# Kernel optimization log

Hardware: AMD Instinct MI355X
Metric: run time of the kernel (lower is better)

Reference implementation:

```python
import jax, jax.numpy as jnp
import numpy as np

D_MODEL, D_STATE, EXPAND = 1024, 128, 2
E = D_MODEL * EXPAND          # 2048
N = D_STATE                   # 128
H = 1
P = E
TD = D_STATE // 2             # 64
Z_DIM = E + E + N + N + H + H + TD + H  # 4369
EPS = 1e-05
B_SZ, L = 4, 2048


def setup_inputs() -> dict:
    key = jax.random.key(0)
    ks = jax.random.split(key, 6)
    u = jax.random.normal(ks[0], (B_SZ, L, D_MODEL), dtype=jnp.float32)
    W_in = jax.random.normal(ks[1], (Z_DIM, D_MODEL), dtype=jnp.float32) * 0.02
    W_out = jax.random.normal(ks[2], (D_MODEL, E), dtype=jnp.float32) * 0.02
    w_normB = jnp.ones((N,), jnp.float32)
    w_normC = jnp.ones((N,), jnp.float32)
    B_bias = jnp.ones((N,), jnp.float32)
    C_bias = jnp.ones((N,), jnp.float32)
    # dt_bias buffer: dt_i ~ logU(0.001, 0.1); dt_bias = dt_i + log(-expm1(-dt_i))
    dt_i = jnp.exp(jax.random.uniform(ks[3], (H,)) * (np.log(0.1) - np.log(0.001)) + np.log(0.001))
    dt_i = jnp.clip(dt_i, 1e-4, None)
    dt_bias = dt_i + jnp.log(-jnp.expm1(-dt_i))
    A_log = jnp.full((H,), np.log(0.5), jnp.float32)
    return {"u": u, "W_in": W_in, "w_normB": w_normB, "w_normC": w_normC,
            "B_bias": B_bias, "C_bias": C_bias, "dt_bias": dt_bias,
            "A_log": A_log, "W_out": W_out}


def _rms(x, w):
    return x * jax.lax.rsqrt(jnp.mean(x * x, axis=-1, keepdims=True) + EPS) * w


def _rope(x, ang):
    half = x.shape[-1] // 2
    x1, x2 = x[..., :half], x[..., half:]
    c, s = jnp.cos(ang), jnp.sin(ang)
    return jnp.concatenate([x1 * c - x2 * s, x1 * s + x2 * c], axis=-1)


def reference(u, W_in, w_normB, w_normC, B_bias, C_bias, dt_bias, A_log, W_out):
    Bb, Ls, _ = u.shape
    z = u @ W_in.T  # [B, L, Z_DIM]
    o = 0
    def take(n):
        nonlocal o
        r = z[..., o:o + n]; o += n; return r
    x = jax.nn.silu(take(E))
    gate = jax.nn.silu(take(E))
    B_ = take(N)
    C_ = take(N)
    dt_ = take(H)
    A_ = take(H)
    th = take(TD)
    lam_ = take(H)

    dt = jax.nn.softplus(dt_ + dt_bias)          # [B, L, H]
    A = -jax.nn.softplus(A_ + A_log)             # [B, L, H]
    lam = jax.nn.sigmoid(lam_)                   # [B, L, H]
    alpha = jnp.exp(dt * A)                      # [B, L, H]

    B_ = _rms(B_, w_normB) + B_bias
    C_ = _rms(C_, w_normC) + C_bias
    ca = jnp.cumsum(jnp.mean(dt, axis=-1, keepdims=True) * th, axis=1)  # [B, L, TD]
    B_ = _rope(B_, ca)
    C_ = _rope(C_, ca)

    xh = x.reshape(Bb, Ls, H, P)
    xp = jnp.concatenate([jnp.zeros_like(xh[:, :1]), xh[:, :-1]], axis=1)  # roll + zero t=0
    lh = lam[..., None]
    xt = lh * xh + (1.0 - lh) * alpha[..., None] * xp  # [B, L, H, P]

    # fallback SSM: per-channel mean drive, per-head scalar A (mean over batch+time)
    u_mean = jnp.mean(xt, axis=-1)               # [B, L, H]
    A_bar = jnp.mean(A, axis=(0, 1))             # [H]
    dA = jnp.exp(dt * A_bar)                     # [B, L, H]
    dBu = dt[..., None] * B_[:, :, None, :] * u_mean[..., None]  # [B, L, H, N]

    def step(state, xs):
        dA_t, dBu_t, C_t = xs                    # [B,H], [B,H,N], [B,N]
        state = dA_t[..., None] * state + dBu_t  # [B, H, N]
        y_t = jnp.einsum('bhn,bn->bh', state, C_t)
        return state, y_t

    state0 = jnp.zeros((Bb, H, N), dtype=xt.dtype)
    _, ys = jax.lax.scan(step, state0,
                         (jnp.moveaxis(dA, 1, 0), jnp.moveaxis(dBu, 1, 0), jnp.moveaxis(C_, 1, 0)))
    outs = jnp.moveaxis(ys, 0, 1)                # [B, L, H]
    y = jnp.broadcast_to(outs, (Bb, Ls, E))      # H=1 expanded to E
    return (y * gate) @ W_out.T
```

## Files before the change

kernel.cpp:

```cpp
#include <hip/hip_runtime.h>
#include <cstdint>
#include <cstddef>

typedef __bf16 bf16_t;
typedef bf16_t bf16x8 __attribute__((ext_vector_type(8)));
typedef bf16_t bf16x4 __attribute__((ext_vector_type(4)));
typedef float f32x4 __attribute__((ext_vector_type(4)));

#define B_SZ    4
#define LSEQ    2048
#define DMODEL  1024
#define EDIM    2048
#define ZDIM    4419
#define ZPAD    4608
#define ROWS    (B_SZ*LSEQ)
#define EPSV    1e-5f

#define LDU     1088
#define LDG     2112

#define SCHUNK  128
#define SCLEN   (LSEQ/SCHUNK)
#define RCH     128
#define RCLEN   (LSEQ/RCH)

__device__ __forceinline__ float softplus_f(float x){
  return fmaxf(x, 0.f) + log1pf(expf(-fabsf(x)));
}
__device__ __forceinline__ float sigmoid_f(float x){ return 1.f/(1.f+expf(-x)); }
__device__ __forceinline__ float silu_f(float x){ return x/(1.f+expf(-x)); }

__device__ __forceinline__ void gload_lds16(const void* g, void* l){
  __builtin_amdgcn_global_load_lds(
      (const __attribute__((address_space(1))) void*)g,
      (__attribute__((address_space(3))) void*)l, 16, 0, 0);
}

__device__ __forceinline__ float blockReduce128(float v, float* red, int t){
  red[t] = v; __syncthreads();
  #pragma unroll
  for (int off = 64; off > 0; off >>= 1){
    if (t < off) red[t] += red[t+off];
    __syncthreads();
  }
  float r = red[0];
  __syncthreads();
  return r;
}

__global__ __launch_bounds__(256) void prep_kernel(
    const float4* __restrict__ u4, const float4* __restrict__ win4,
    const float4* __restrict__ wout4,
    bf16_t* __restrict__ ubf, bf16_t* __restrict__ winSh, bf16_t* __restrict__ woutSh,
    float* __restrict__ Asum, float* __restrict__ xraw)
{
  size_t i = (size_t)blockIdx.x*256 + threadIdx.x;
  if (i == 0) Asum[0] = 0.f;
  if (i < ROWS) xraw[i] = 0.f;
  const size_t NU4 = (size_t)ROWS*DMODEL/4;
  const size_t NW4 = (size_t)ZPAD*DMODEL/4;
  const size_t NO4 = (size_t)DMODEL*EDIM/4;
  if (i < NU4){
    float4 v = u4[i];
    size_t e = i*4, row = e>>10, col = e&1023;
    bf16x4 o = { (bf16_t)v.x, (bf16_t)v.y, (bf16_t)v.z, (bf16_t)v.w };
    *(bf16x4*)&ubf[row*LDU + col] = o;
    return;
  }
  i -= NU4;
  if (i < NW4){
    size_t e = i*4, row = e>>10, k = e&1023;
    bf16x4 o;
    if (row < (size_t)ZDIM){
      float4 v = win4[i];
      o = bf16x4{ (bf16_t)v.x, (bf16_t)v.y, (bf16_t)v.z, (bf16_t)v.w };
    } else {
      o = bf16x4{ (bf16_t)0.f, (bf16_t)0.f, (bf16_t)0.f, (bf16_t)0.f };
    }
    int ntile = (int)(row>>4), colf = (int)(row&15);
    int kt = (int)(k>>5), koct = (int)((k>>3)&3), ko = (int)(k&7);
    size_t off = (((size_t)ntile*32 + kt)<<9) + (koct<<7) + (colf<<3) + ko;
    *(bf16x4*)&winSh[off] = o;
    return;
  }
  i -= NW4;
  if (i < NO4){
    float4 v = wout4[i];
    size_t e = i*4, row = e>>11, k = e&2047;
    bf16x4 o = { (bf16_t)v.x, (bf16_t)v.y, (bf16_t)v.z, (bf16_t)v.w };
    int ntile = (int)(row>>4), colf = (int)(row&15);
    int kt = (int)(k>>5), koct = (int)((k>>3)&3), ko = (int)(k&7);
    size_t off = (((size_t)ntile*64 + kt)<<9) + (koct<<7) + (colf<<3) + ko;
    *(bf16x4*)&woutSh[off] = o;
  }
}

template<int LDA_, int NKT, int NT, int NXT, int MODE>
__global__ __launch_bounds__(256, 2) void gemmV_kernel(
    const bf16_t* __restrict__ A0, const bf16_t* __restrict__ Bsh,
    float* __restrict__ xraw, bf16_t* __restrict__ o_g, float* __restrict__ o_z,
    const float* __restrict__ scale, float* __restrict__ o_f)
{
  __shared__ __align__(16) bf16_t lds[8192];

  const int tid = threadIdx.x;
  const int wid = tid>>6, lane = tid&63;
  const int wr = wid>>1, wc = wid&1;
  const int lr = lane&15, hi = lane>>4;

  constexpr int MB = ROWS/128;
  constexpr int NWG = NXT*MB;
  const int id = blockIdx.x;
  const int rid = (id & 7)*(NWG/8) + (id>>3);
  const int bx = rid % NXT, by = rid / NXT;
  const int m0 = by*128, n0 = bx*256;

  f32x4 acc[4][8] = {};

  const bf16_t* pA0; const bf16_t* pA1;
  int dA0, dA1;
  {
    int c0 = tid,      r0 = c0>>2, d0 = c0&3, g0 = (d0 - (r0>>1)) & 3;
    int c1 = 256+tid,  r1 = c1>>2, d1 = c1&3, g1 = (d1 - (r1>>1)) & 3;
    pA0 = A0 + (size_t)(m0+r0)*LDA_ + g0*8;
    pA1 = A0 + (size_t)(m0+r1)*LDA_ + g1*8;
    dA0 = c0*8; dA1 = c1*8;
  }
  int aoff[4];
  {
    int R0 = wr*64 + lr;
    int cA = (hi + (R0>>1)) & 3;
    #pragma unroll
    for (int m = 0; m < 4; ++m) aoff[m] = (R0 + 16*m)*32 + cA*8;
  }
  const bf16_t* bB0 = Bsh + (((size_t)((n0>>4) + wc*8)*NKT)<<9) + lane*8;
  int koff = 0;

  bf16x8 bA[8], bB[8], af[4];

  gload_lds16(pA0, &lds[dA0]); pA0 += 32;
  gload_lds16(pA1, &lds[dA1]); pA1 += 32;
  #pragma unroll
  for (int n = 0; n < 8; ++n)
    bA[n] = *(const bf16x8*)(bB0 + (size_t)n*(NKT*512) + koff);
  koff += 512;
  asm volatile("s_waitcnt vmcnt(8)" ::: "memory");
  __builtin_amdgcn_s_barrier();

  #pragma unroll 1
  for (int t2 = 0; t2 < NT/2; ++t2){
    {
      #pragma unroll
      for (int m = 0; m < 4; ++m) af[m] = *(const bf16x8*)&lds[aoff[m]];
      gload_lds16(pA0, &lds[4096 + dA0]); pA0 += 32;
      gload_lds16(pA1, &lds[4096 + dA1]); pA1 += 32;
      #pragma unroll
      for (int n = 0; n < 8; ++n)
        bB[n] = *(const bf16x8*)(bB0 + (size_t)n*(NKT*512) + koff);
      koff += 512;
      #pragma unroll
      for (int m = 0; m < 4; ++m)
        #pragma unroll
        for (int n = 0; n < 8; ++n)
          acc[m][n] = __builtin_amdgcn_mfma_f32_16x16x32_bf16(af[m], bA[n], acc[m][n], 0,0,0);
      asm volatile("s_waitcnt vmcnt(8)" ::: "memory");
      __builtin_amdgcn_s_barrier();
    }
    {
      #pragma unroll
      for (int m = 0; m < 4; ++m) af[m] = *(const bf16x8*)&lds[4096 + aoff[m]];
      const bool pf = (t2 < NT/2 - 1);
      if (pf){
        gload_lds16(pA0, &lds[dA0]); pA0 += 32;
        gload_lds16(pA1, &lds[dA1]); pA1 += 32;
        #pragma unroll
        for (int n = 0; n < 8; ++n)
          bA[n] = *(const bf16x8*)(bB0 + (size_t)n*(NKT*512) + koff);
        koff += 512;
      }
      #pragma unroll
      for (int m = 0; m < 4; ++m)
        #pragma unroll
        for (int n = 0; n < 8; ++n)
          acc[m][n] = __builtin_amdgcn_mfma_f32_16x16x32_bf16(af[m], bB[n], acc[m][n], 0,0,0);
      if (pf) { asm volatile("s_waitcnt vmcnt(8)" ::: "memory"); }
      else    { asm volatile("s_waitcnt vmcnt(0)" ::: "memory"); }
      __builtin_amdgcn_s_barrier();
    }
  }

  if (MODE == 0 && n0 < 2048){
    #pragma unroll
    for (int m = 0; m < 4; ++m){
      #pragma unroll
      for (int i = 0; i < 4; ++i){
        float p = 0.f;
        #pragma unroll
        for (int n = 0; n < 8; ++n) p += silu_f(acc[m][n][i]);
        p += __shfl_xor(p, 8); p += __shfl_xor(p, 4);
        p += __shfl_xor(p, 2); p += __shfl_xor(p, 1);
        if (lr == 0){
          int r = m0 + wr*64 + m*16 + (hi<<2) + i;
          atomicAdd(xraw + r, p);
        }
      }
    }
  } else if (MODE == 0){
    #pragma unroll
    for (int m = 0; m < 4; ++m){
      int rowb = m0 + wr*64 + m*16 + (hi<<2);
      #pragma unroll
      for (int n = 0; n < 8; ++n){
        int col = n0 + wc*128 + n*16 + lr;
        #pragma unroll
        for (int i = 0; i < 4; ++i){
          int r = rowb + i;
          float v = acc[m][n][i];
          if (col < 4096)      o_g[(size_t)r*LDG + (col-2048)] = (bf16_t)silu_f(v);
          else if (col < 4480) o_z[(size_t)r*384 + (col-4096)] = v;
        }
      }
    }
  } else {
    #pragma unroll
    for (int m = 0; m < 4; ++m){
      int rowb = m0 + wr*64 + m*16 + (hi<<2);
      #pragma unroll
      for (int i = 0; i < 4; ++i){
        int r = rowb + i;
        float s = scale[r];
        #pragma unroll
        for (int n = 0; n < 8; ++n){
          int col = n0 + wc*128 + n*16 + lr;
          o_f[(size_t)r*DMODEL + col] = acc[m][n][i]*s;
        }
      }
    }
  }
}

__global__ __launch_bounds__(128) void fuse_kernel(
    const float* __restrict__ xraw, const float* __restrict__ zs,
    const float* __restrict__ wnB, const float* __restrict__ wnC,
    const float* __restrict__ Bb, const float* __restrict__ Cb,
    const float* __restrict__ dtb, const float* __restrict__ Alog,
    float* __restrict__ Bn, float* __restrict__ Cn, float* __restrict__ dtth,
    float* __restrict__ dts, float* __restrict__ alphas, float* __restrict__ lams,
    float* __restrict__ xbar, float* Asum)
{
  __shared__ float red[128];
  int r = blockIdx.x, t = threadIdx.x;
  const float* zr = zs + (size_t)r*384;
  float bv = zr[t], cv = zr[128+t];
  float b2 = blockReduce128(bv*bv, red, t);
  float c2 = blockReduce128(cv*cv, red, t);
  float rb = rsqrtf(b2*(1.f/128.f) + EPSV);
  float rc = rsqrtf(c2*(1.f/128.f) + EPSV);
  Bn[(size_t)r*128 + t] = bv*rb*wnB[t] + Bb[t];
  Cn[(size_t)r*128 + t] = cv*rc*wnC[t] + Cb[t];

  float dt = softplus_f(zr[256] + dtb[0]);
  if (t < 64) dtth[(size_t)r*64 + t] = dt * zr[258+t];
  if (t == 0){
    float Av  = -softplus_f(zr[257] + Alog[0]);
    float lam = sigmoid_f(zr[322]);
    dts[r]    = dt;
    alphas[r] = expf(dt*Av);
    lams[r]   = lam;
    xbar[r]   = xraw[r] * (1.f/2048.f);
    atomicAdd(Asum, Av);
  }
}

__global__ __launch_bounds__(64) void rope_sum_kernel(
    const float* __restrict__ dtth, float* __restrict__ csum)
{
  int b  = blockIdx.x >> 7;
  int ch = blockIdx.x & 127;
  int d  = threadIdx.x;
  const float* base = dtth + ((size_t)b*LSEQ + (size_t)ch*RCLEN)*64 + d;
  float s = 0.f;
  #pragma unroll
  for (int i = 0; i < RCLEN; ++i) s += base[(size_t)i*64];
  csum[((size_t)b*RCH + ch)*64 + d] = s;
}

__global__ __launch_bounds__(64) void rope_prefix_kernel(float* __restrict__ csum)
{
  int b = blockIdx.x, d = threadIdx.x;
  float s = 0.f;
  for (int c = 0; c < RCH; ++c){
    size_t idx = ((size_t)b*RCH + c)*64 + d;
    float v = csum[idx]; csum[idx] = s; s += v;
  }
}

__global__ __launch_bounds__(64) void rope_scan_kernel(
    const float* __restrict__ dtth, const float* __restrict__ csum,
    const float* __restrict__ dts, const float* __restrict__ alphas,
    const float* __restrict__ lams, const float* __restrict__ xbar,
    const float* __restrict__ Asum,
    const float* __restrict__ Bn, float* __restrict__ Cn,
    float* __restrict__ ylocal, float* __restrict__ Pfix,
    float* __restrict__ Sfin, float* __restrict__ Dch)
{
  int b  = blockIdx.x >> 7;
  int ch = blockIdx.x & 127;
  int d  = threadIdx.x;
  float Abar = Asum[0] * (1.f/(float)ROWS);
  float ca = csum[((size_t)b*RCH + ch)*64 + d];
  float s1 = 0.f, s2 = 0.f, P = 1.f;
  int l0 = ch*SCLEN;
  #pragma unroll
  for (int i = 0; i < SCLEN; ++i){
    int l = l0 + i;
    size_t r = (size_t)b*LSEQ + l;
    ca += dtth[r*64 + d];
    float sn, cs;
    sincosf(ca, &sn, &cs);
    size_t ro = r*128;
    float b1 = Bn[ro+d], b2v = Bn[ro+64+d];
    float rb1 = b1*cs - b2v*sn;
    float rb2 = b1*sn + b2v*cs;
    float c1 = Cn[ro+d], c2v = Cn[ro+64+d];
    float rc1 = c1*cs - c2v*sn;
    float rc2 = c1*sn + c2v*cs;
    Cn[ro+d]    = rc1;
    Cn[ro+64+d] = rc2;

    float dt = dts[r], lam = lams[r], al = alphas[r], xb = xbar[r];
    float xp = (l > 0) ? xbar[r-1] : 0.f;
    float um = lam*xb + (1.f-lam)*al*xp;
    float dA = expf(dt*Abar);
    float coef = dt*um;
    s1 = dA*s1 + coef*rb1;
    s2 = dA*s2 + coef*rb2;
    P *= dA;
    float p = s1*rc1 + s2*rc2;
    #pragma unroll
    for (int off = 32; off > 0; off >>= 1) p += __shfl_down(p, off);
    if (d == 0){ ylocal[r] = p; Pfix[r] = P; }
  }
  size_t so = ((size_t)b*SCHUNK + ch)*128;
  Sfin[so + d]      = s1;
  Sfin[so + 64 + d] = s2;
  if (d == 0) Dch[b*SCHUNK + ch] = P;
}

__global__ __launch_bounds__(128) void scan_carry_kernel(
    const float* __restrict__ Sfin, const float* __restrict__ Dch,
    float* __restrict__ Sin)
{
  int b = blockIdx.x;
  int n = threadIdx.x;
  float s = 0.f;
  for (int c = 0; c < SCHUNK; ++c){
    size_t so = ((size_t)b*SCHUNK + c)*128;
    Sin[so + n] = s;
    s = Dch[b*SCHUNK + c]*s + Sfin[so + n];
  }
}

__global__ __launch_bounds__(256) void scan_fix_kernel(
    const float* __restrict__ Cn, const float* __restrict__ Sin,
    const float* __restrict__ ylocal, const float* __restrict__ Pfix,
    float* __restrict__ outsv)
{
  int r = blockIdx.x*4 + (threadIdx.x>>6);
  int n = threadIdx.x & 63;
  int b  = r / LSEQ;
  int ch = (r % LSEQ) / SCLEN;
  const float* si = Sin + ((size_t)b*SCHUNK + ch)*128;
  size_t ro = (size_t)r*128;
  float p = Cn[ro+n]*si[n] + Cn[ro+64+n]*si[64+n];
  #pragma unroll
  for (int off = 32; off > 0; off >>= 1) p += __shfl_down(p, off);
  if (n == 0) outsv[r] = ylocal[r] + Pfix[r]*p;
}

extern "C" void kernel_launch(void* const* d_in, const int* in_sizes, int n_in,
                              void* d_out, int out_size, void* d_ws, size_t ws_size,
                              hipStream_t stream)
{
  const float* u    = (const float*)d_in[0];
  const float* W_in = (const float*)d_in[1];
  const float* wnB  = (const float*)d_in[2];
  const float* wnC  = (const float*)d_in[3];
  const float* Bb   = (const float*)d_in[4];
  const float* Cb   = (const float*)d_in[5];
  const float* dtb  = (const float*)d_in[6];
  const float* Alog = (const float*)d_in[7];
  const float* Wout = (const float*)d_in[8];
  float* out = (float*)d_out;
  char* ws = (char*)d_ws;

  constexpr size_t OFF_ASUM = 0;
  constexpr size_t OFF_UBF  = 256;
  constexpr size_t SZ_UBF   = (size_t)ROWS*LDU*2;
  constexpr size_t OFF_WIN  = OFF_UBF + SZ_UBF;
  constexpr size_t SZ_WIN   = (size_t)ZPAD*LDU*2;
  constexpr size_t OFF_WOUT = OFF_WIN + SZ_WIN;
  constexpr size_t SZ_WOUT  = (size_t)DMODEL*LDG*2;
  constexpr size_t OFF_G    = OFF_WOUT + SZ_WOUT;
  constexpr size_t SZ_G     = (size_t)ROWS*LDG*2;
  constexpr size_t OFF_ZS   = OFF_G + SZ_G;
  constexpr size_t SZ_ZS    = (size_t)ROWS*384*4;
  constexpr size_t OFF_BN   = OFF_ZS + SZ_ZS;
  constexpr size_t SZ_BN    = (size_t)ROWS*128*4;
  constexpr size_t OFF_CN   = OFF_BN + SZ_BN;
  constexpr size_t OFF_DTTH = OFF_CN + SZ_BN;
  constexpr size_t SZ_DTTH  = (size_t)ROWS*64*4;
  constexpr size_t OFF_XRAW = OFF_DTTH + SZ_DTTH;
  constexpr size_t OFF_DT   = OFF_XRAW + (size_t)ROWS*4;
  constexpr size_t OFF_AL   = OFF_DT  + (size_t)ROWS*4;
  constexpr size_t OFF_LAM  = OFF_AL  + (size_t)ROWS*4;
  constexpr size_t OFF_XB   = OFF_LAM + (size_t)ROWS*4;
  constexpr size_t OFF_OUTS = OFF_XB  + (size_t)ROWS*4;
  constexpr size_t OFF_YLOC = OFF_OUTS + (size_t)ROWS*4;
  constexpr size_t OFF_PFIX = OFF_YLOC + (size_t)ROWS*4;
  constexpr size_t OFF_SFIN = OFF_PFIX + (size_t)ROWS*4;
  constexpr size_t SZ_SFIN  = (size_t)B_SZ*SCHUNK*128*4;
  constexpr size_t OFF_DCH  = OFF_SFIN + SZ_SFIN;
  constexpr size_t OFF_SIN  = OFF_DCH + (size_t)B_SZ*SCHUNK*4;
  constexpr size_t OFF_CSUM = OFF_SIN + SZ_SFIN;

  float*  Asum   = (float*) (ws + OFF_ASUM);
  bf16_t* ubf    = (bf16_t*)(ws + OFF_UBF);
  bf16_t* winSh  = (bf16_t*)(ws + OFF_WIN);
  bf16_t* woutSh = (bf16_t*)(ws + OFF_WOUT);
  bf16_t* gbuf   = (bf16_t*)(ws + OFF_G);
  float*  zsb    = (float*) (ws + OFF_ZS);
  float*  Bn     = (float*) (ws + OFF_BN);
  float*  Cn     = (float*) (ws + OFF_CN);
  float*  dtth   = (float*) (ws + OFF_DTTH);
  float*  xraw   = (float*) (ws + OFF_XRAW);
  float*  dts    = (float*) (ws + OFF_DT);
  float*  alphas = (float*) (ws + OFF_AL);
  float*  lams   = (float*) (ws + OFF_LAM);
  float*  xbar   = (float*) (ws + OFF_XB);
  float*  outsv  = (float*) (ws + OFF_OUTS);
  float*  ylocal = (float*) (ws + OFF_YLOC);
  float*  Pfix   = (float*) (ws + OFF_PFIX);
  float*  Sfin   = (float*) (ws + OFF_SFIN);
  float*  Dch    = (float*) (ws + OFF_DCH);
  float*  Sin    = (float*) (ws + OFF_SIN);
  float*  csum   = (float*) (ws + OFF_CSUM);

  {
    size_t total4 = ((size_t)ROWS*DMODEL + (size_t)ZPAD*DMODEL + (size_t)DMODEL*EDIM)/4;
    int blocks = (int)((total4 + 255)/256);
    prep_kernel<<<blocks, 256, 0, stream>>>(
        (const float4*)u, (const float4*)W_in, (const float4*)Wout,
        ubf, winSh, woutSh, Asum, xraw);
  }

  gemmV_kernel<LDU, 32, 32, ZPAD/256, 0>
      <<<(ZPAD/256)*(ROWS/128), 256, 0, stream>>>(
      ubf, winSh, xraw, gbuf, zsb, nullptr, nullptr);
  fuse_kernel<<<ROWS, 128, 0, stream>>>(xraw, zsb, wnB, wnC, Bb, Cb, dtb, Alog,
                                        Bn, Cn, dtth, dts, alphas, lams, xbar, Asum);
  rope_sum_kernel<<<B_SZ*RCH, 64, 0, stream>>>(dtth, csum);
  rope_prefix_kernel<<<B_SZ, 64, 0, stream>>>(csum);
  rope_scan_kernel<<<B_SZ*RCH, 64, 0, stream>>>(dtth, csum, dts, alphas, lams,
                                                xbar, Asum, Bn, Cn,
                                                ylocal, Pfix, Sfin, Dch);
  scan_carry_kernel<<<B_SZ, 128, 0, stream>>>(Sfin, Dch, Sin);
  scan_fix_kernel<<<ROWS/4, 256, 0, stream>>>(Cn, Sin, ylocal, Pfix, outsv);
  gemmV_kernel<LDG, 64, 64, DMODEL/256, 1>
      <<<(DMODEL/256)*(ROWS/128), 256, 0, stream>>>(
      gbuf, woutSh, nullptr, nullptr, nullptr, outsv, out);
}
```

Baseline: 342.8 us.

## Pre-swizzle u into MFMA fragment layout and load A directly to registers

The prep kernel now writes u in bf16 in the same tiled fragment layout already used for W_in, so each lane's 16-byte A fragment sits contiguously in global memory. A new gemmD kernel for the input projection loads both A and B fragments straight into registers with double buffering, dropping the LDS staging, the waitcnt calls and the barriers. This removes LDS traffic and synchronisation, but each wave now fetches its own A fragments from global/L2 memory and there is no explicit cross-wave sharing of A tiles. The output projection keeps the original LDS-based kernel.

```diff
diff --git a/kernel.cpp b/kernel.cpp
--- a/kernel.cpp
+++ b/kernel.cpp
@@ -51,7 +51,7 @@
 __global__ __launch_bounds__(256) void prep_kernel(
     const float4* __restrict__ u4, const float4* __restrict__ win4,
     const float4* __restrict__ wout4,
-    bf16_t* __restrict__ ubf, bf16_t* __restrict__ winSh, bf16_t* __restrict__ woutSh,
+    bf16_t* __restrict__ uSh, bf16_t* __restrict__ winSh, bf16_t* __restrict__ woutSh,
     float* __restrict__ Asum, float* __restrict__ xraw)
 {
   size_t i = (size_t)blockIdx.x*256 + threadIdx.x;
@@ -62,9 +62,12 @@
   const size_t NO4 = (size_t)DMODEL*EDIM/4;
   if (i < NU4){
     float4 v = u4[i];
-    size_t e = i*4, row = e>>10, col = e&1023;
+    size_t e = i*4, row = e>>10, k = e&1023;
     bf16x4 o = { (bf16_t)v.x, (bf16_t)v.y, (bf16_t)v.z, (bf16_t)v.w };
-    *(bf16x4*)&ubf[row*LDU + col] = o;
+    int mt = (int)(row>>4), rowf = (int)(row&15);
+    int kt = (int)(k>>5), koct = (int)((k>>3)&3), ko = (int)(k&7);
+    size_t off = (((size_t)mt*32 + kt)<<9) + (koct<<7) + (rowf<<3) + ko;
+    *(bf16x4*)&uSh[off] = o;
     return;
   }
   i -= NU4;
@@ -95,14 +98,11 @@
   }
 }
 
-template<int LDA_, int NKT, int NT, int NXT, int MODE>
-__global__ __launch_bounds__(256, 2) void gemmV_kernel(
-    const bf16_t* __restrict__ A0, const bf16_t* __restrict__ Bsh,
-    float* __restrict__ xraw, bf16_t* __restrict__ o_g, float* __restrict__ o_z,
-    const float* __restrict__ scale, float* __restrict__ o_f)
-{
-  __shared__ __align__(16) bf16_t lds[8192];
-
+template<int NKT, int NT, int NXT>
+__global__ __launch_bounds__(256, 2) void gemmD_kernel(
+    const bf16_t* __restrict__ Ash, const bf16_t* __restrict__ Bsh,
+    float* __restrict__ xraw, bf16_t* __restrict__ o_g, float* __restrict__ o_z)
+{
   const int tid = threadIdx.x;
   const int wid = tid>>6, lane = tid&63;
   const int wr = wid>>1, wc = wid&1;
@@ -116,80 +116,46 @@
   const int m0 = by*128, n0 = bx*256;
 
   f32x4 acc[4][8] = {};
-
-  const bf16_t* pA0; const bf16_t* pA1;
-  int dA0, dA1;
-  {
-    int c0 = tid,      r0 = c0>>2, d0 = c0&3, g0 = (d0 - (r0>>1)) & 3;
-    int c1 = 256+tid,  r1 = c1>>2, d1 = c1&3, g1 = (d1 - (r1>>1)) & 3;
-    pA0 = A0 + (size_t)(m0+r0)*LDA_ + g0*8;
-    pA1 = A0 + (size_t)(m0+r1)*LDA_ + g1*8;
-    dA0 = c0*8; dA1 = c1*8;
-  }
-  int aoff[4];
-  {
-    int R0 = wr*64 + lr;
-    int cA = (hi + (R0>>1)) & 3;
-    #pragma unroll
-    for (int m = 0; m < 4; ++m) aoff[m] = (R0 + 16*m)*32 + cA*8;
-  }
-  const bf16_t* bB0 = Bsh + (((size_t)((n0>>4) + wc*8)*NKT)<<9) + lane*8;
+  constexpr size_t TS = (size_t)NKT*512;
+  const bf16_t* pa = Ash + ((size_t)((m0>>4) + wr*4)*NKT<<9) + lane*8;
+  const bf16_t* pb = Bsh + ((size_t)((n0>>4) + wc*8)*NKT<<9) + lane*8;
+
+  bf16x8 aA[4], aB[4], bA[8], bB[8];
   int koff = 0;
-
-  bf16x8 bA[8], bB[8], af[4];
-
-  gload_lds16(pA0, &lds[dA0]); pA0 += 32;
-  gload_lds16(pA1, &lds[dA1]); pA1 += 32;
-  #pragma unroll
-  for (int n = 0; n < 8; ++n)
-    bA[n] = *(const bf16x8*)(bB0 + (size_t)n*(NKT*512) + koff);
+  #pragma unroll
+  for (int m=0;m<4;++m) aA[m] = *(const bf16x8*)(pa + m*TS + koff);
+  #pragma unroll
+  for (int n=0;n<8;++n) bA[n] = *(const bf16x8*)(pb + n*TS + koff);
   koff += 512;
-  asm volatile("s_waitcnt vmcnt(8)" ::: "memory");
-  __builtin_amdgcn_s_barrier();
 
   #pragma unroll 1
   for (int t2 = 0; t2 < NT/2; ++t2){
-    {
-      #pragma unroll
-      for (int m = 0; m < 4; ++m) af[m] = *(const bf16x8*)&lds[aoff[m]];
-      gload_lds16(pA0, &lds[4096 + dA0]); pA0 += 32;
-      gload_lds16(pA1, &lds[4096 + dA1]); pA1 += 32;
-      #pragma unroll
-      for (int n = 0; n < 8; ++n)
-        bB[n] = *(const bf16x8*)(bB0 + (size_t)n*(NKT*512) + koff);
+    #pragma unroll
+    for (int m=0;m<4;++m) aB[m] = *(const bf16x8*)(pa + m*TS + koff);
+    #pragma unroll
+    for (int n=0;n<8;++n) bB[n] = *(const bf16x8*)(pb + n*TS + koff);
+    koff += 512;
+    #pragma unroll
+    for (int m=0;m<4;++m)
+      #pragma unroll
+      for (int n=0;n<8;++n)
+        acc[m][n] = __builtin_amdgcn_mfma_f32_16x16x32_bf16(aA[m], bA[n], acc[m][n], 0,0,0);
+    const bool pf = (t2 < NT/2 - 1);
+    if (pf){
+      #pragma unroll
+      for (int m=0;m<4;++m) aA[m] = *(const bf16x8*)(pa + m*TS + koff);
+      #pragma unroll
+      for (int n=0;n<8;++n) bA[n] = *(const bf16x8*)(pb + n*TS + koff);
       koff += 512;
-      #pragma unroll
-      for (int m = 0; m < 4; ++m)
-        #pragma unroll
-        for (int n = 0; n < 8; ++n)
-          acc[m][n] = __builtin_amdgcn_mfma_f32_16x16x32_bf16(af[m], bA[n], acc[m][n], 0,0,0);
-      asm volatile("s_waitcnt vmcnt(8)" ::: "memory");
-      __builtin_amdgcn_s_barrier();
-    }
-    {
-      #pragma unroll
-      for (int m = 0; m < 4; ++m) af[m] = *(const bf16x8*)&lds[4096 + aoff[m]];
-      const bool pf = (t2 < NT/2 - 1);
-      if (pf){
-        gload_lds16(pA0, &lds[dA0]); pA0 += 32;
-        gload_lds16(pA1, &lds[dA1]); pA1 += 32;
-        #pragma unroll
-        for (int n = 0; n < 8; ++n)
-          bA[n] = *(const bf16x8*)(bB0 + (size_t)n*(NKT*512) + koff);
-        koff += 512;
-      }
-      #pragma unroll
-      for (int m = 0; m < 4; ++m)
-        #pragma unroll
-        for (int n = 0; n < 8; ++n)
-          acc[m][n] = __builtin_amdgcn_mfma_f32_16x16x32_bf16(af[m], bB[n], acc[m][n], 0,0,0);
-      if (pf) { asm volatile("s_waitcnt vmcnt(8)" ::: "memory"); }
-      else    { asm volatile("s_waitcnt vmcnt(0)" ::: "memory"); }
-      __builtin_amdgcn_s_barrier();
-    }
-  }
-
-  if (MODE == 0 && n0 < 2048){
+    }
+    #pragma unroll
+    for (int m=0;m<4;++m)
+      #pragma unroll
+      for (int n=0;n<8;++n)
+        acc[m][n] = __builtin_amdgcn_mfma_f32_16x16x32_bf16(aB[m], bB[n], acc[m][n], 0,0,0);
+  }
+
+  if (n0 < 2048){
     #pragma unroll
     for (int m = 0; m < 4; ++m){
       #pragma unroll
@@ -205,7 +171,7 @@
         }
       }
     }
-  } else if (MODE == 0){
+  } else {
     #pragma unroll
     for (int m = 0; m < 4; ++m){
       int rowb = m0 + wr*64 + m*16 + (hi<<2);
@@ -221,19 +187,113 @@
         }
       }
     }
-  } else {
-    #pragma unroll
-    for (int m = 0; m < 4; ++m){
-      int rowb = m0 + wr*64 + m*16 + (hi<<2);
-      #pragma unroll
-      for (int i = 0; i < 4; ++i){
-        int r = rowb + i;
-        float s = scale[r];
+  }
+}
+
+template<int LDA_, int NKT, int NT, int NXT>
+__global__ __launch_bounds__(256, 2) void gemmV_kernel(
+    const bf16_t* __restrict__ A0, const bf16_t* __restrict__ Bsh,
+    const float* __restrict__ scale, float* __restrict__ o_f)
+{
+  __shared__ __align__(16) bf16_t lds[8192];
+
+  const int tid = threadIdx.x;
+  const int wid = tid>>6, lane = tid&63;
+  const int wr = wid>>1, wc = wid&1;
+  const int lr = lane&15, hi = lane>>4;
+
+  constexpr int MB = ROWS/128;
+  constexpr int NWG = NXT*MB;
+  const int id = blockIdx.x;
+  const int rid = (id & 7)*(NWG/8) + (id>>3);
+  const int bx = rid % NXT, by = rid / NXT;
+  const int m0 = by*128, n0 = bx*256;
+
+  f32x4 acc[4][8] = {};
+
+  const bf16_t* pA0; const bf16_t* pA1;
+  int dA0, dA1;
+  {
+    int c0 = tid,      r0 = c0>>2, d0 = c0&3, g0 = (d0 - (r0>>1)) & 3;
+    int c1 = 256+tid,  r1 = c1>>2, d1 = c1&3, g1 = (d1 - (r1>>1)) & 3;
+    pA0 = A0 + (size_t)(m0+r0)*LDA_ + g0*8;
+    pA1 = A0 + (size_t)(m0+r1)*LDA_ + g1*8;
+    dA0 = c0*8; dA1 = c1*8;
+  }
+  int aoff[4];
+  {
+    int R0 = wr*64 + lr;
+    int cA = (hi + (R0>>1)) & 3;
+    #pragma unroll
+    for (int m = 0; m < 4; ++m) aoff[m] = (R0 + 16*m)*32 + cA*8;
+  }
+  const bf16_t* bB0 = Bsh + (((size_t)((n0>>4) + wc*8)*NKT)<<9) + lane*8;
+  int koff = 0;
+
+  bf16x8 bA[8], bB[8], af[4];
+
+  gload_lds16(pA0, &lds[dA0]); pA0 += 32;
+  gload_lds16(pA1, &lds[dA1]); pA1 += 32;
+  #pragma unroll
+  for (int n = 0; n < 8; ++n)
+    bA[n] = *(const bf16x8*)(bB0 + (size_t)n*(NKT*512) + koff);
+  koff += 512;
+  asm volatile("s_waitcnt vmcnt(8)" ::: "memory");
+  __builtin_amdgcn_s_barrier();
+
+  #pragma unroll 1
+  for (int t2 = 0; t2 < NT/2; ++t2){
+    {
+      #pragma unroll
+      for (int m = 0; m < 4; ++m) af[m] = *(const bf16x8*)&lds[aoff[m]];
+      gload_lds16(pA0, &lds[4096 + dA0]); pA0 += 32;
+      gload_lds16(pA1, &lds[4096 + dA1]); pA1 += 32;
+      #pragma unroll
+      for (int n = 0; n < 8; ++n)
+        bB[n] = *(const bf16x8*)(bB0 + (size_t)n*(NKT*512) + koff);
+      koff += 512;
+      #pragma unroll
+      for (int m = 0; m < 4; ++m)
         #pragma unroll
-        for (int n = 0; n < 8; ++n){
-          int col = n0 + wc*128 + n*16 + lr;
-          o_f[(size_t)r*DMODEL + col] = acc[m][n][i]*s;
-        }
+        for (int n = 0; n < 8; ++n)
+          acc[m][n] = __builtin_amdgcn_mfma_f32_16x16x32_bf16(af[m], bA[n], acc[m][n], 0,0,0);
+      asm volatile("s_waitcnt vmcnt(8)" ::: "memory");
+      __builtin_amdgcn_s_barrier();
+    }
+    {
+      #pragma unroll
+      for (int m = 0; m < 4; ++m) af[m] = *(const bf16x8*)&lds[4096 + aoff[m]];
+      const bool pf = (t2 < NT/2 - 1);
+      if (pf){
+        gload_lds16(pA0, &lds[dA0]); pA0 += 32;
+        gload_lds16(pA1, &lds[dA1]); pA1 += 32;
+        #pragma unroll
+        for (int n = 0; n < 8; ++n)
+          bA[n] = *(const bf16x8*)(bB0 + (size_t)n*(NKT*512) + koff);
+        koff += 512;
+      }
+      #pragma unroll
+      for (int m = 0; m < 4; ++m)
+        #pragma unroll
+        for (int n = 0; n < 8; ++n)
+          acc[m][n] = __builtin_amdgcn_mfma_f32_16x16x32_bf16(af[m], bB[n], acc[m][n], 0,0,0);
+      if (pf) { asm volatile("s_waitcnt vmcnt(8)" ::: "memory"); }
+      else    { asm volatile("s_waitcnt vmcnt(0)" ::: "memory"); }
+      __builtin_amdgcn_s_barrier();
+    }
+  }
+
+  #pragma unroll
+  for (int m = 0; m < 4; ++m){
+    int rowb = m0 + wr*64 + m*16 + (hi<<2);
+    #pragma unroll
+    for (int i = 0; i < 4; ++i){
+      int r = rowb + i;
+      float s = scale[r];
+      #pragma unroll
+      for (int n = 0; n < 8; ++n){
+        int col = n0 + wc*128 + n*16 + lr;
+        o_f[(size_t)r*DMODEL + col] = acc[m][n][i]*s;
       }
     }
   }
@@ -425,7 +485,7 @@
   constexpr size_t OFF_CSUM = OFF_SIN + SZ_SFIN;
 
   float*  Asum   = (float*) (ws + OFF_ASUM);
-  bf16_t* ubf    = (bf16_t*)(ws + OFF_UBF);
+  bf16_t* uSh    = (bf16_t*)(ws + OFF_UBF);
   bf16_t* winSh  = (bf16_t*)(ws + OFF_WIN);
   bf16_t* woutSh = (bf16_t*)(ws + OFF_WOUT);
   bf16_t* gbuf   = (bf16_t*)(ws + OFF_G);
@@ -451,12 +511,12 @@
     int blocks = (int)((total4 + 255)/256);
     prep_kernel<<<blocks, 256, 0, stream>>>(
         (const float4*)u, (const float4*)W_in, (const float4*)Wout,
-        ubf, winSh, woutSh, Asum, xraw);
-  }
-
-  gemmV_kernel<LDU, 32, 32, ZPAD/256, 0>
+        uSh, winSh, woutSh, Asum, xraw);
+  }
+
+  gemmD_kernel<32, 32, ZPAD/256>
       <<<(ZPAD/256)*(ROWS/128), 256, 0, stream>>>(
-      ubf, winSh, xraw, gbuf, zsb, nullptr, nullptr);
+      uSh, winSh, xraw, gbuf, zsb);
   fuse_kernel<<<ROWS, 128, 0, stream>>>(xraw, zsb, wnB, wnC, Bb, Cb, dtb, Alog,
                                         Bn, Cn, dtth, dts, alphas, lams, xbar, Asum);
   rope_sum_kernel<<<B_SZ*RCH, 64, 0, stream>>>(dtth, csum);
@@ -466,7 +526,7 @@
                                                 ylocal, Pfix, Sfin, Dch);
   scan_carry_kernel<<<B_SZ, 128, 0, stream>>>(Sfin, Dch, Sin);
   scan_fix_kernel<<<ROWS/4, 256, 0, stream>>>(Cn, Sin, ylocal, Pfix, outsv);
-  gemmV_kernel<LDG, 64, 64, DMODEL/256, 1>
+  gemmV_kernel<LDG, 64, 64, DMODEL/256>
       <<<(DMODEL/256)*(ROWS/128), 256, 0, stream>>>(
-      gbuf, woutSh, nullptr, nullptr, nullptr, outsv, out);
-}
+      gbuf, woutSh, outsv, out);
+}
```

Result: no change. 337.6 us (-1.5%).
